# Kernel tuning notes

Measured on AMD Instinct MI355X. Metric: run time of the kernel, lower is better.

The kernel has to match this reference:

```python
import jax, jax.numpy as jnp
import numpy as np

USER_NUM = 100000
ITEM_NUM = 50000
N = USER_NUM + ITEM_NUM
D = 64
NNZ = 2400000
B = 4096
NLEVEL = 3
LEAF = 32
HID = 256
NCLS = 2
NLAYERS = 2
EPS = 0.1
TAU = 0.2


def _l2norm(x, axis=-1):
    return x / jnp.clip(jnp.linalg.norm(x, axis=axis, keepdims=True), 1e-12)


def setup_inputs():
    key = jax.random.key(0)
    ks = jax.random.split(key, 32)
    def w(k, shape):
        fan = shape[-2] if len(shape) >= 2 else shape[-1]
        return jax.random.normal(k, shape, jnp.float32) / np.sqrt(fan)
    z = lambda *s: jnp.zeros(s, jnp.float32)
    return {
        "ego_emb": w(ks[0], (N, D)),
        "gc_w": w(ks[1], (NLAYERS, D, D)), "gc_b": z(NLAYERS, D),
        "bi_w": w(ks[2], (NLAYERS, D, D)), "bi_b": z(NLAYERS, D),
        "uh_w": w(ks[3], (NLEVEL, D, D)), "uh_b": z(NLEVEL, D),
        "ih_w": w(ks[4], (NLEVEL, D, D)), "ih_b": z(NLEVEL, D),
        "ud_w1": w(ks[5], (NLEVEL, D, HID)), "ud_b1": z(NLEVEL, HID),
        "ud_w2": w(ks[6], (NLEVEL, HID, LEAF)), "ud_b2": z(NLEVEL, LEAF),
        "id_w1": w(ks[7], (NLEVEL, D, HID)), "id_b1": z(NLEVEL, HID),
        "id_w2": w(ks[8], (NLEVEL, HID, LEAF)), "id_b2": z(NLEVEL, LEAF),
        "q_w": w(ks[9], (LEAF, LEAF)), "q_b": z(LEAF),
        "k_w": w(ks[10], (LEAF, LEAF)), "k_b": z(LEAF),
        "v_w": w(ks[11], (LEAF, LEAF)), "v_b": z(LEAF),
        "dg_w1": w(ks[12], (NLEVEL * LEAF, D)), "dg_b1": z(D),
        "dg_w2": w(ks[13], (D, D)), "dg_b2": z(D),
        "pr_w": w(ks[14], (D, NCLS)), "pr_b": z(NCLS),
        "adj_vals": jax.random.uniform(ks[15], (NNZ,), jnp.float32) / 16.0,
        "hier_skills": jax.random.uniform(ks[16], (B, NLEVEL * LEAF), jnp.float32),
        "user_id": jax.random.randint(ks[17], (B,), 0, USER_NUM),
        "item_id": jax.random.randint(ks[18], (B,), 0, ITEM_NUM),
        "adj_rows": jax.random.randint(ks[19], (NNZ,), 0, N),
        "adj_cols": jax.random.randint(ks[20], (NNZ,), 0, N),
    }


def _sam(x, q_w, q_b, k_w, k_b, v_w, v_b):
    # x: [B, S, d], single-head self-attention (n_heads=1)
    d = x.shape[-1]
    q = x @ q_w + q_b
    k = x @ k_w + k_b
    v = x @ v_w + v_b
    scores = jnp.einsum('bsd,btd->bst', q, k) / jnp.sqrt(jnp.float32(d))
    attn = jax.nn.softmax(scores, axis=-1)  # softmax over key axis t
    return jnp.einsum('bst,btd->bsd', attn, v)


def _cl_loss(v1, v2):
    n1 = _l2norm(v1)
    n2 = _l2norm(v2)
    pos = jnp.exp(jnp.sum(n1 * n2, -1) / TAU)
    ttl = jnp.sum(jnp.exp(n1 @ n2.T / TAU), axis=1)
    return jnp.mean(-jnp.log(pos / ttl))


def _cl_module(recs, key):
    # recs: [L, B, LEAF]
    noise = jax.random.uniform(key, recs.shape, recs.dtype)
    recs_new = recs + jnp.sign(recs) * _l2norm(noise) * EPS
    return jnp.mean(jax.vmap(_cl_loss)(recs, recs_new))


def reference(ego_emb, gc_w, gc_b, bi_w, bi_b, uh_w, uh_b, ih_w, ih_b,
              ud_w1, ud_b1, ud_w2, ud_b2, id_w1, id_b1, id_w2, id_b2,
              q_w, q_b, k_w, k_b, v_w, v_b, dg_w1, dg_b1, dg_w2, dg_b2,
              pr_w, pr_b, adj_vals, hier_skills, user_id, item_id,
              adj_rows, adj_cols):
    # ---- NGCF propagation: sparse adj matmul + bi-interaction ----
    E = ego_emb
    E_sum = ego_emb
    for l in range(NLAYERS):
        side = jax.ops.segment_sum(adj_vals[:, None] * E[adj_cols], adj_rows,
                                   num_segments=N)  # spmm(adj_norm, E)
        sum_e = jax.nn.leaky_relu(side @ gc_w[l] + gc_b[l])
        bi_e = jax.nn.leaky_relu((E * side) @ bi_w[l] + bi_b[l])
        E = _l2norm(sum_e + bi_e)  # dropout -> identity (eval)
        E_sum = E_sum + E
    ue = E_sum[:USER_NUM][user_id]   # [B, D]
    ie = E_sum[USER_NUM:][item_id]   # [B, D]
    # ---- hierarchy projections + disentangled encoders (stacked over levels) ----
    u_reps = jnp.tanh(jnp.einsum('bd,lde->lbe', ue, uh_w) + uh_b[:, None, :])
    i_reps = jnp.tanh(jnp.einsum('bd,lde->lbe', ie, ih_w) + ih_b[:, None, :])
    u_recs = jnp.einsum('lbh,lhk->lbk',
                        jnp.tanh(jnp.einsum('lbd,ldh->lbh', u_reps, ud_w1) + ud_b1[:, None, :]),
                        ud_w2) + ud_b2[:, None, :]  # [L, B, LEAF]
    i_recs = jnp.einsum('lbh,lhk->lbk',
                        jnp.tanh(jnp.einsum('lbd,ldh->lbh', i_reps, id_w1) + id_b1[:, None, :]),
                        id_w2) + id_b2[:, None, :]
    # ---- self-attention across levels ----
    u_att = _sam(u_recs.transpose(1, 0, 2), q_w, q_b, k_w, k_b, v_w, v_b)  # [B, L, LEAF]
    i_att = _sam(i_recs.transpose(1, 0, 2), q_w, q_b, k_w, k_b, v_w, v_b)
    # ---- contrastive losses (detached in original via torch.Tensor(...)) ----
    kc = jax.random.split(jax.random.key(42), 2)
    cl = _cl_module(u_att.transpose(1, 0, 2), kc[0]) + _cl_module(i_att.transpose(1, 0, 2), kc[1])
    cl = jax.lax.stop_gradient(cl)
    # ---- diagnosis head ----
    skills = hier_skills.reshape(B, NLEVEL, LEAF)
    diag = ((jax.nn.sigmoid(u_att) - jax.nn.sigmoid(i_att)) * skills).reshape(B, NLEVEL * LEAF)
    h = jnp.tanh(diag @ dg_w1 + dg_b1) @ dg_w2 + dg_b2  # dropout -> identity (eval)
    out = jax.nn.softmax(h @ pr_w + pr_b, axis=-1)
    return (out, cl)
```

## Files before the change

kernel.cpp:

```cpp
#include <hip/hip_runtime.h>
#include <stdint.h>
#include <math.h>

#define USER_N 100000
#define NODE_N 150000
#define DD 64
#define NNZE 2400000
#define BB 4096
#define NLV 3
#define LF 32
#define HALF_SZ 196608u
#define NTILE 586
#define NSUB 8
#define SCAP 1024
#define EPB 4096

typedef __attribute__((ext_vector_type(8))) short bf16x8;
typedef __attribute__((ext_vector_type(4))) float f32x4;
typedef __attribute__((ext_vector_type(2))) float f32x2;

#define XCC_ID_IMM 63508

__host__ __device__ inline void tf_block(uint32_t k0, uint32_t k1, uint32_t& x0, uint32_t& x1) {
  uint32_t ks[3] = {k0, k1, k0 ^ k1 ^ 0x1BD11BDAu};
  x0 += ks[0]; x1 += ks[1];
  const int R0[4] = {13, 15, 26, 6};
  const int R1[4] = {17, 29, 16, 24};
#pragma unroll
  for (int i = 0; i < 5; ++i) {
    const int* R = (i & 1) ? R1 : R0;
#pragma unroll
    for (int j = 0; j < 4; ++j) {
      x0 += x1;
      x1 = (x1 << R[j]) | (x1 >> (32 - R[j]));
      x1 ^= x0;
    }
    x0 += ks[(i + 1) % 3];
    x1 += ks[(i + 2) % 3] + (uint32_t)(i + 1);
  }
}

__device__ inline float tf_uniform(uint32_t ka, uint32_t kb, uint32_t m) {
  uint32_t x0, x1;
  bool first = m < HALF_SZ;
  if (first) { x0 = m; x1 = m + HALF_SZ; } else { x0 = m - HALF_SZ; x1 = m; }
  tf_block(ka, kb, x0, x1);
  uint32_t bits = first ? x0 : x1;
  return __uint_as_float((bits >> 9) | 0x3f800000u) - 1.0f;
}

__device__ inline unsigned short f2bf(float x) {
  uint32_t b = __float_as_uint(x);
  return (unsigned short)((b + 0x7FFFu + ((b >> 16) & 1u)) >> 16);
}

__device__ inline unsigned char f2fp8(float x) {
  return (unsigned char)(__builtin_amdgcn_cvt_pk_fp8_f32(x, x, 0, false) & 0xFF);
}

__device__ inline void fp8_fma(float4& acc, uint2 rec, uint32_t wrd) {
  float vv = __uint_as_float(rec.y);
  f32x2 lo = __builtin_amdgcn_cvt_pk_f32_fp8((int)wrd, false);
  f32x2 hi = __builtin_amdgcn_cvt_pk_f32_fp8((int)wrd, true);
  acc.x = fmaf(vv, lo.x, acc.x);
  acc.y = fmaf(vv, lo.y, acc.y);
  acc.z = fmaf(vv, hi.x, acc.z);
  acc.w = fmaf(vv, hi.y, acc.w);
}

__global__ __launch_bounds__(256) void k_init(const float* __restrict__ ego,
                                              uint32_t* __restrict__ E8) {
  int i = blockIdx.x * 256 + threadIdx.x;
  float4 v = ((const float4*)ego)[i];
  int w01 = __builtin_amdgcn_cvt_pk_fp8_f32(v.x, v.y, 0, false);
  int w = __builtin_amdgcn_cvt_pk_fp8_f32(v.z, v.w, w01, true);
  E8[i] = (uint32_t)w;
}

__global__ __launch_bounds__(256) void k_wprep(
    const float* __restrict__ uh_w, const float* __restrict__ ud_w1,
    const float* __restrict__ ud_w2, const float* __restrict__ ih_w,
    const float* __restrict__ id_w1, const float* __restrict__ id_w2,
    unsigned short* __restrict__ s1t, unsigned short* __restrict__ s2t,
    unsigned short* __restrict__ s3t) {
  int i = blockIdx.x * 256 + threadIdx.x;
  if (i < 24576) {
    int sl = i >> 12, r = i & 4095, e = r >> 6, d = r & 63;
    const float* src = (sl >= 3 ? ih_w : uh_w);
    int l = sl % 3;
    s1t[i] = f2bf(src[l * 4096 + d * 64 + e]);
  } else if (i < 24576 + 98304) {
    int j = i - 24576;
    int sl = j >> 14, r = j & 16383, e = r >> 6, d = r & 63;
    const float* src = (sl >= 3 ? id_w1 : ud_w1);
    int l = sl % 3;
    s2t[j] = f2bf(src[l * 16384 + d * 256 + e]);
  } else if (i < 172032) {
    int j = i - 24576 - 98304;
    int sl = j >> 13, r = j & 8191, e = r >> 8, d = r & 255;
    const float* src = (sl >= 3 ? id_w2 : ud_w2);
    int l = sl % 3;
    s3t[j] = f2bf(src[l * 8192 + d * 32 + e]);
  }
}

__global__ __launch_bounds__(256) void k_scatter_t(const int* __restrict__ rows,
                                                   const int* __restrict__ cols,
                                                   const float* __restrict__ vals,
                                                   int* __restrict__ cursor,
                                                   uint2* __restrict__ sedge_r) {
  __shared__ int cnt[NTILE];
  __shared__ int curs[NTILE];
  int t = threadIdx.x;
  for (int i = t; i < NTILE; i += 256) cnt[i] = 0;
  __syncthreads();
  int r[16];
  int ebase = blockIdx.x * EPB;
#pragma unroll
  for (int j = 0; j < 16; ++j) {
    int e = ebase + j * 256 + t;
    r[j] = (e < NNZE) ? rows[e] : -1;
    if (r[j] >= 0) atomicAdd(&cnt[r[j] >> 8], 1);
  }
  __syncthreads();
  unsigned myx = __builtin_amdgcn_s_getreg(XCC_ID_IMM) & (NSUB - 1);
  for (int i = t; i < NTILE; i += 256) {
    int c = cnt[i];
    curs[i] = c ? atomicAdd(&cursor[(i * NSUB + (int)myx) * 16], c) : 0;
  }
  __syncthreads();
#pragma unroll
  for (int j = 0; j < 16; ++j) {
    if (r[j] < 0) continue;
    int e = ebase + j * 256 + t;
    int tile = r[j] >> 8;
    uint2 rec = make_uint2((uint32_t)cols[e] | ((uint32_t)(r[j] & 255) << 18),
                           __float_as_uint(vals[e]));
    int p = atomicAdd(&curs[tile], 1);
    if (p < SCAP) {
      sedge_r[(size_t)(tile * NSUB + (int)myx) * SCAP + p] = rec;
    } else {
#pragma unroll 1
      for (int att = 1; att < NSUB; ++att) {
        int seg = tile * NSUB + (int)((myx + att) & (NSUB - 1));
        int p2 = atomicAdd(&cursor[seg * 16], 1);
        if (p2 < SCAP) { sedge_r[(size_t)seg * SCAP + p2] = rec; break; }
      }
    }
  }
}

__global__ __launch_bounds__(1024) void k_scan586(const int* __restrict__ cursor,
                                                  int* __restrict__ out_base,
                                                  int* __restrict__ row_start) {
  __shared__ int buf[1024];
  int t = threadIdx.x;
  int tot = 0;
  if (t < NTILE) {
#pragma unroll
    for (int x = 0; x < NSUB; ++x) {
      int c = cursor[(t * NSUB + x) * 16];
      tot += (c < SCAP) ? c : SCAP;
    }
  }
  buf[t] = tot;
  __syncthreads();
  for (int off = 1; off < 1024; off <<= 1) {
    int add = (t >= off) ? buf[t - off] : 0;
    __syncthreads();
    buf[t] += add;
    __syncthreads();
  }
  if (t < NTILE) out_base[t] = buf[t] - tot;
  if (t == 0) row_start[NODE_N] = NNZE;
}

__global__ __launch_bounds__(256) void k_sort_t(const uint2* __restrict__ sedge_r,
                                                const int* __restrict__ cursor,
                                                const int* __restrict__ out_base,
                                                uint2* __restrict__ sedge,
                                                int* __restrict__ row_start) {
  __shared__ int hist[256], buf[256], curs[256];
  int t = threadIdx.x;
  int tile = blockIdx.x;
  int obase = out_base[tile];
  hist[t] = 0;
  __syncthreads();
#pragma unroll 1
  for (int x = 0; x < NSUB; ++x) {
    int seg = tile * NSUB + x;
    int cnt = cursor[seg * 16];
    if (cnt > SCAP) cnt = SCAP;
    const uint2* sp = sedge_r + (size_t)seg * SCAP;
    for (int i = t; i < cnt; i += 256)
      atomicAdd(&hist[sp[i].x >> 18], 1);
  }
  __syncthreads();
  int v = hist[t];
  buf[t] = v;
  __syncthreads();
  for (int off = 1; off < 256; off <<= 1) {
    int add = (t >= off) ? buf[t - off] : 0;
    __syncthreads();
    buf[t] += add;
    __syncthreads();
  }
  int excl = buf[t] - v;
  curs[t] = excl;
  int row = tile * 256 + t;
  if (row < NODE_N) row_start[row] = obase + excl;
  __syncthreads();
#pragma unroll 1
  for (int x = 0; x < NSUB; ++x) {
    int seg = tile * NSUB + x;
    int cnt = cursor[seg * 16];
    if (cnt > SCAP) cnt = SCAP;
    const uint2* sp = sedge_r + (size_t)seg * SCAP;
    for (int i = t; i < cnt; i += 256) {
      uint2 rec = sp[i];
      int rl = rec.x >> 18;
      int p = atomicAdd(&curs[rl], 1);
      sedge[obase + p] = make_uint2(rec.x & 0x3FFFFu, rec.y);
    }
  }
}

__global__ __launch_bounds__(256) void k_spmm(const uint32_t* __restrict__ E8,
                                              const uint2* __restrict__ sedge,
                                              const int* __restrict__ row_start,
                                              unsigned short* __restrict__ side16,
                                              unsigned short* __restrict__ p16) {
  int r = blockIdx.x * 4 + (threadIdx.x >> 6);
  int lane = threadIdx.x & 63;
  int g = lane >> 4;
  int q = lane & 15;
  int rs = row_start[r], re = row_start[r + 1];
  float4 acc = make_float4(0.f, 0.f, 0.f, 0.f);
  int e = rs;
  for (; e + 16 <= re; e += 16) {
    uint2 e0 = sedge[e + g];
    uint2 e1 = sedge[e + 4 + g];
    uint2 e2 = sedge[e + 8 + g];
    uint2 e3 = sedge[e + 12 + g];
    uint32_t a0 = E8[(size_t)e0.x * 16 + q];
    uint32_t a1 = E8[(size_t)e1.x * 16 + q];
    uint32_t a2 = E8[(size_t)e2.x * 16 + q];
    uint32_t a3 = E8[(size_t)e3.x * 16 + q];
    fp8_fma(acc, e0, a0);
    fp8_fma(acc, e1, a1);
    fp8_fma(acc, e2, a2);
    fp8_fma(acc, e3, a3);
  }
  for (; e + 8 <= re; e += 8) {
    uint2 e0 = sedge[e + g];
    uint2 e1 = sedge[e + 4 + g];
    uint32_t a0 = E8[(size_t)e0.x * 16 + q];
    uint32_t a1 = E8[(size_t)e1.x * 16 + q];
    fp8_fma(acc, e0, a0);
    fp8_fma(acc, e1, a1);
  }
  for (; e + 4 <= re; e += 4) {
    uint2 e0 = sedge[e + g];
    uint32_t a0 = E8[(size_t)e0.x * 16 + q];
    fp8_fma(acc, e0, a0);
  }
  for (; e < re; ++e) {
    if (g == (e & 3)) {
      uint2 e0 = sedge[e];
      uint32_t a0 = E8[(size_t)e0.x * 16 + q];
      fp8_fma(acc, e0, a0);
    }
  }
#pragma unroll
  for (int off = 16; off <= 32; off <<= 1) {
    acc.x += __shfl_xor(acc.x, off, 64);
    acc.y += __shfl_xor(acc.y, off, 64);
    acc.z += __shfl_xor(acc.z, off, 64);
    acc.w += __shfl_xor(acc.w, off, 64);
  }
  if (g == 0) {
    uint32_t ew = E8[(size_t)r * 16 + q];
    f32x2 elo = __builtin_amdgcn_cvt_pk_f32_fp8((int)ew, false);
    f32x2 ehi = __builtin_amdgcn_cvt_pk_f32_fp8((int)ew, true);
    ushort4 s16, pp;
    s16.x = f2bf(acc.x); s16.y = f2bf(acc.y); s16.z = f2bf(acc.z); s16.w = f2bf(acc.w);
    pp.x = f2bf(acc.x * elo.x); pp.y = f2bf(acc.y * elo.y);
    pp.z = f2bf(acc.z * ehi.x); pp.w = f2bf(acc.w * ehi.y);
    *(ushort4*)&side16[(size_t)r * DD + q * 4] = s16;
    *(ushort4*)&p16[(size_t)r * DD + q * 4] = pp;
  }
}

__global__ __launch_bounds__(256) void k_transform(const float* __restrict__ gw,
                                                   const float* __restrict__ gb,
                                                   const float* __restrict__ bw,
                                                   const float* __restrict__ bb,
                                                   const unsigned short* __restrict__ side16,
                                                   const unsigned short* __restrict__ p16,
                                                   float* __restrict__ Eout,
                                                   unsigned char* __restrict__ E8b) {
  int t = threadIdx.x;
  int wv = t >> 6, lane = t & 63;
  int n = lane & 15, quad = lane >> 4;
  bf16x8 wg[4][2], wb[4][2];
  float gbl[4], bbl[4];
#pragma unroll
  for (int c = 0; c < 4; ++c) {
    gbl[c] = gb[c * 16 + n];
    bbl[c] = bb[c * 16 + n];
#pragma unroll
    for (int h = 0; h < 2; ++h) {
#pragma unroll
      for (int j = 0; j < 8; ++j) {
        int k = h * 32 + quad * 8 + j;
        wg[c][h][j] = (short)f2bf(gw[k * 64 + c * 16 + n]);
        wb[c][h][j] = (short)f2bf(bw[k * 64 + c * 16 + n]);
      }
    }
  }
  const f32x4 z = {0.f, 0.f, 0.f, 0.f};
  for (int tile = blockIdx.x * 4 + wv; tile < NODE_N / 16; tile += gridDim.x * 4) {
    int i0 = tile * 16;
    bf16x8 as0 = *(const bf16x8*)&side16[(size_t)(i0 + n) * DD + quad * 8];
    bf16x8 as1 = *(const bf16x8*)&side16[(size_t)(i0 + n) * DD + 32 + quad * 8];
    bf16x8 ap0 = *(const bf16x8*)&p16[(size_t)(i0 + n) * DD + quad * 8];
    bf16x8 ap1 = *(const bf16x8*)&p16[(size_t)(i0 + n) * DD + 32 + quad * 8];
    float v[4][4];
    float sq0 = 0.f, sq1 = 0.f, sq2 = 0.f, sq3 = 0.f;
#pragma unroll
    for (int c = 0; c < 4; ++c) {
      f32x4 ag = __builtin_amdgcn_mfma_f32_16x16x32_bf16(as0, wg[c][0], z, 0, 0, 0);
      ag = __builtin_amdgcn_mfma_f32_16x16x32_bf16(as1, wg[c][1], ag, 0, 0, 0);
      f32x4 ab = __builtin_amdgcn_mfma_f32_16x16x32_bf16(ap0, wb[c][0], z, 0, 0, 0);
      ab = __builtin_amdgcn_mfma_f32_16x16x32_bf16(ap1, wb[c][1], ab, 0, 0, 0);
#pragma unroll
      for (int r = 0; r < 4; ++r) {
        float a1 = ag[r] + gbl[c];
        a1 = (a1 > 0.f) ? a1 : 0.01f * a1;
        float a2 = ab[r] + bbl[c];
        a2 = (a2 > 0.f) ? a2 : 0.01f * a2;
        float vv = a1 + a2;
        v[c][r] = vv;
        if (r == 0) sq0 += vv * vv;
        else if (r == 1) sq1 += vv * vv;
        else if (r == 2) sq2 += vv * vv;
        else sq3 += vv * vv;
      }
    }
#pragma unroll
    for (int off = 1; off < 16; off <<= 1) {
      sq0 += __shfl_xor(sq0, off, 64);
      sq1 += __shfl_xor(sq1, off, 64);
      sq2 += __shfl_xor(sq2, off, 64);
      sq3 += __shfl_xor(sq3, off, 64);
    }
    float inv0 = 1.f / fmaxf(sqrtf(sq0), 1e-12f);
    float inv1 = 1.f / fmaxf(sqrtf(sq1), 1e-12f);
    float inv2 = 1.f / fmaxf(sqrtf(sq2), 1e-12f);
    float inv3 = 1.f / fmaxf(sqrtf(sq3), 1e-12f);
#pragma unroll
    for (int c = 0; c < 4; ++c) {
      float vn0 = v[c][0] * inv0;
      float vn1 = v[c][1] * inv1;
      float vn2 = v[c][2] * inv2;
      float vn3 = v[c][3] * inv3;
      size_t o0 = (size_t)(i0 + quad * 4 + 0) * DD + c * 16 + n;
      size_t o1 = o0 + DD, o2 = o1 + DD, o3 = o2 + DD;
      Eout[o0] = vn0; Eout[o1] = vn1; Eout[o2] = vn2; Eout[o3] = vn3;
      E8b[o0] = f2fp8(vn0); E8b[o1] = f2fp8(vn1);
      E8b[o2] = f2fp8(vn2); E8b[o3] = f2fp8(vn3);
    }
  }
}

__global__ __launch_bounds__(128) void k_gather(const float* __restrict__ ego,
                                                const float* __restrict__ E1,
                                                const float* __restrict__ E2,
                                                const int* __restrict__ uid,
                                                const int* __restrict__ iid,
                                                unsigned short* __restrict__ ue16,
                                                unsigned short* __restrict__ ie16) {
  int b = blockIdx.x, t = threadIdx.x;
  if (t < 64) {
    size_t o = (size_t)uid[b] * 64 + t;
    ue16[(size_t)b * 64 + t] = f2bf(ego[o] + E1[o] + E2[o]);
  } else {
    int d = t - 64;
    size_t o = (size_t)(USER_N + iid[b]) * 64 + d;
    ie16[(size_t)b * 64 + d] = f2bf(ego[o] + E1[o] + E2[o]);
  }
}

__global__ __launch_bounds__(256) void k_encoder5(
    const unsigned short* __restrict__ ue16, const unsigned short* __restrict__ ie16,
    const unsigned short* __restrict__ s1t, const unsigned short* __restrict__ s2t,
    const unsigned short* __restrict__ s3t,
    const float* __restrict__ uh_b, const float* __restrict__ ud_b1,
    const float* __restrict__ ud_b2, const float* __restrict__ ih_b,
    const float* __restrict__ id_b1, const float* __restrict__ id_b2,
    float* __restrict__ recs_u, float* __restrict__ recs_i) {
  __shared__ unsigned short R1[32][64];
  __shared__ unsigned short T[32][256];
  int t = threadIdx.x;
  int w = t >> 6, lane = t & 63;
  int n = lane & 15, quad = lane >> 4;
  int trow = w & 1;
  int cg = w >> 1;
  int r0 = blockIdx.x * 32;
  int l = blockIdx.y, side = blockIdx.z;
  int sl = side * 3 + l;
  const unsigned short* x16 = side ? ie16 : ue16;
  const float* hb = side ? ih_b : uh_b;
  const float* bb1 = side ? id_b1 : ud_b1;
  const float* bb2 = side ? id_b2 : ud_b2;
  float* recs = side ? recs_i : recs_u;
  const f32x4 z = {0.f, 0.f, 0.f, 0.f};

  {
    const unsigned short* xr = &x16[(size_t)(r0 + trow * 16 + n) * 64];
    bf16x8 a0 = *(const bf16x8*)&xr[quad * 8];
    bf16x8 a1 = *(const bf16x8*)&xr[32 + quad * 8];
    const unsigned short* Wt = s1t + (size_t)sl * 4096;
#pragma unroll
    for (int cc = 0; cc < 2; ++cc) {
      int cb = cg * 2 + cc;
      bf16x8 wb0 = *(const bf16x8*)&Wt[(size_t)(cb * 16 + n) * 64 + quad * 8];
      bf16x8 wb1 = *(const bf16x8*)&Wt[(size_t)(cb * 16 + n) * 64 + 32 + quad * 8];
      f32x4 acc = __builtin_amdgcn_mfma_f32_16x16x32_bf16(a0, wb0, z, 0, 0, 0);
      acc = __builtin_amdgcn_mfma_f32_16x16x32_bf16(a1, wb1, acc, 0, 0, 0);
      float bias = hb[l * 64 + cb * 16 + n];
#pragma unroll
      for (int r = 0; r < 4; ++r)
        R1[trow * 16 + quad * 4 + r][cb * 16 + n] = f2bf(tanhf(acc[r] + bias));
    }
  }
  __syncthreads();

  {
    bf16x8 a0 = *(const bf16x8*)&R1[trow * 16 + n][quad * 8];
    bf16x8 a1 = *(const bf16x8*)&R1[trow * 16 + n][32 + quad * 8];
    const unsigned short* Wt = s2t + (size_t)sl * 16384;
#pragma unroll
    for (int cc = 0; cc < 8; ++cc) {
      int cb = cg * 8 + cc;
      bf16x8 wb0 = *(const bf16x8*)&Wt[(size_t)(cb * 16 + n) * 64 + quad * 8];
      bf16x8 wb1 = *(const bf16x8*)&Wt[(size_t)(cb * 16 + n) * 64 + 32 + quad * 8];
      f32x4 acc = __builtin_amdgcn_mfma_f32_16x16x32_bf16(a0, wb0, z, 0, 0, 0);
      acc = __builtin_amdgcn_mfma_f32_16x16x32_bf16(a1, wb1, acc, 0, 0, 0);
      float bias = bb1[l * 256 + cb * 16 + n];
#pragma unroll
      for (int r = 0; r < 4; ++r)
        T[trow * 16 + quad * 4 + r][cb * 16 + n] = f2bf(tanhf(acc[r] + bias));
    }
  }
  __syncthreads();

  {
    const unsigned short* Wt = s3t + (size_t)sl * 8192;
    f32x4 acc = z;
#pragma unroll
    for (int h = 0; h < 8; ++h) {
      bf16x8 a = *(const bf16x8*)&T[trow * 16 + n][h * 32 + quad * 8];
      bf16x8 b = *(const bf16x8*)&Wt[(size_t)(cg * 16 + n) * 256 + h * 32 + quad * 8];
      acc = __builtin_amdgcn_mfma_f32_16x16x32_bf16(a, b, acc, 0, 0, 0);
    }
    float bias = bb2[l * 32 + cg * 16 + n];
#pragma unroll
    for (int r = 0; r < 4; ++r)
      recs[((size_t)l * BB + (r0 + trow * 16 + quad * 4 + r)) * 32 + cg * 16 + n] =
          acc[r] + bias;
  }
}

__global__ __launch_bounds__(256) void k_attn(const float* __restrict__ recs,
                                              const float* __restrict__ qw, const float* __restrict__ qb,
                                              const float* __restrict__ kw, const float* __restrict__ kb,
                                              const float* __restrict__ vw, const float* __restrict__ vb,
                                              float* __restrict__ att) {
  int t = threadIdx.x;
  int b = blockIdx.x * 8 + (t >> 5);
  int d = t & 31;
  float x0 = recs[((size_t)0 * BB + b) * 32 + d];
  float x1 = recs[((size_t)1 * BB + b) * 32 + d];
  float x2 = recs[((size_t)2 * BB + b) * 32 + d];
  float q0 = qb[d], q1 = q0, q2 = q0;
  float c0 = kb[d], c1 = c0, c2 = c0;
  float v0 = vb[d], v1 = v0, v2 = v0;
#pragma unroll 4
  for (int kk = 0; kk < 32; ++kk) {
    float xa = __shfl(x0, kk, 32);
    float xb = __shfl(x1, kk, 32);
    float xc = __shfl(x2, kk, 32);
    float wq = qw[kk * 32 + d], wk = kw[kk * 32 + d], wv = vw[kk * 32 + d];
    q0 += xa * wq; q1 += xb * wq; q2 += xc * wq;
    c0 += xa * wk; c1 += xb * wk; c2 += xc * wk;
    v0 += xa * wv; v1 += xb * wv; v2 += xc * wv;
  }
  float qs[3] = {q0, q1, q2}, ks[3] = {c0, c1, c2}, vs[3] = {v0, v1, v2};
  float sc[3][3];
#pragma unroll
  for (int s = 0; s < 3; ++s)
#pragma unroll
    for (int u = 0; u < 3; ++u) {
      float p = qs[s] * ks[u];
#pragma unroll
      for (int off = 16; off; off >>= 1) p += __shfl_xor(p, off, 32);
      sc[s][u] = p * 0.17677669529663687f;
    }
#pragma unroll
  for (int s = 0; s < 3; ++s) {
    float m = fmaxf(sc[s][0], fmaxf(sc[s][1], sc[s][2]));
    float e0 = __expf(sc[s][0] - m), e1 = __expf(sc[s][1] - m), e2 = __expf(sc[s][2] - m);
    float inv = 1.f / (e0 + e1 + e2);
    att[(size_t)b * 96 + s * 32 + d] = (e0 * vs[0] + e1 * vs[1] + e2 * vs[2]) * inv;
  }
}

__global__ __launch_bounds__(256) void k_noise(const float* __restrict__ att_u,
                                               const float* __restrict__ att_i,
                                               uint32_t ku0, uint32_t ku1, uint32_t ki0, uint32_t ki1,
                                               unsigned short* __restrict__ n1b,
                                               unsigned short* __restrict__ n2b,
                                               float* __restrict__ posdot) {
  int t = threadIdx.x;
  int g = blockIdx.x * 8 + (t >> 5);
  int k = t & 31;
  int side = g / (NLV * BB);
  int rem = g - side * (NLV * BB);
  int l = rem >> 12;
  int b = rem & 4095;
  const float* att = side ? att_i : att_u;
  uint32_t ka = side ? ki0 : ku0;
  uint32_t kb = side ? ki1 : ku1;
  float r = att[(size_t)b * 96 + l * 32 + k];
  float ss = r * r;
#pragma unroll
  for (int off = 16; off; off >>= 1) ss += __shfl_xor(ss, off, 32);
  float v1 = r / fmaxf(sqrtf(ss), 1e-12f);
  uint32_t m = ((uint32_t)(l * BB + b)) * 32u + (uint32_t)k;
  float u = tf_uniform(ka, kb, m);
  float us = u * u;
#pragma unroll
  for (int off = 16; off; off >>= 1) us += __shfl_xor(us, off, 32);
  float un = u / fmaxf(sqrtf(us), 1e-12f);
  float sgn = (r > 0.f) ? 1.f : ((r < 0.f) ? -1.f : 0.f);
  float rn = r + sgn * un * 0.1f;
  float s2 = rn * rn;
#pragma unroll
  for (int off = 16; off; off >>= 1) s2 += __shfl_xor(s2, off, 32);
  float v2 = rn / fmaxf(sqrtf(s2), 1e-12f);
  float pd = v1 * v2;
#pragma unroll
  for (int off = 16; off; off >>= 1) pd += __shfl_xor(pd, off, 32);
  size_t o = (size_t)g * 32 + k;
  n1b[o] = f2bf(v1);
  n2b[o] = f2bf(v2);
  if (k == 0) posdot[g] = pd;
}

__global__ __launch_bounds__(256) void k_ttl(const unsigned short* __restrict__ n1b,
                                             const unsigned short* __restrict__ n2b,
                                             float* __restrict__ ttl) {
  int t = threadIdx.x;
  int wv = t >> 6, lane = t & 63;
  int sl = blockIdx.x >> 6;
  int istripe = blockIdx.x & 63;
  int i0 = istripe * 64 + wv * 16;
  const unsigned short* ab = n1b + (size_t)sl * BB * 32;
  const unsigned short* bb = n2b + (size_t)sl * BB * 32;
  int m = lane & 15, quad = lane >> 4;
  bf16x8 afrag = *(const bf16x8*)&ab[(size_t)(i0 + m) * 32 + quad * 8];
  float r0a = 0.f, r1a = 0.f, r2a = 0.f, r3a = 0.f;
  f32x4 z = {0.f, 0.f, 0.f, 0.f};
  for (int jt = 0; jt < 256; jt += 4) {
    bf16x8 b0 = *(const bf16x8*)&bb[((size_t)((jt + 0) * 16 + m)) * 32 + quad * 8];
    bf16x8 b1 = *(const bf16x8*)&bb[((size_t)((jt + 1) * 16 + m)) * 32 + quad * 8];
    bf16x8 b2 = *(const bf16x8*)&bb[((size_t)((jt + 2) * 16 + m)) * 32 + quad * 8];
    bf16x8 b3 = *(const bf16x8*)&bb[((size_t)((jt + 3) * 16 + m)) * 32 + quad * 8];
    f32x4 s0 = __builtin_amdgcn_mfma_f32_16x16x32_bf16(afrag, b0, z, 0, 0, 0);
    f32x4 s1 = __builtin_amdgcn_mfma_f32_16x16x32_bf16(afrag, b1, z, 0, 0, 0);
    f32x4 s2 = __builtin_amdgcn_mfma_f32_16x16x32_bf16(afrag, b2, z, 0, 0, 0);
    f32x4 s3 = __builtin_amdgcn_mfma_f32_16x16x32_bf16(afrag, b3, z, 0, 0, 0);
    r0a += __expf(s0.x * 5.f) + __expf(s1.x * 5.f) + __expf(s2.x * 5.f) + __expf(s3.x * 5.f);
    r1a += __expf(s0.y * 5.f) + __expf(s1.y * 5.f) + __expf(s2.y * 5.f) + __expf(s3.y * 5.f);
    r2a += __expf(s0.z * 5.f) + __expf(s1.z * 5.f) + __expf(s2.z * 5.f) + __expf(s3.z * 5.f);
    r3a += __expf(s0.w * 5.f) + __expf(s1.w * 5.f) + __expf(s2.w * 5.f) + __expf(s3.w * 5.f);
  }
#pragma unroll
  for (int off = 1; off < 16; off <<= 1) {
    r0a += __shfl_xor(r0a, off, 64);
    r1a += __shfl_xor(r1a, off, 64);
    r2a += __shfl_xor(r2a, off, 64);
    r3a += __shfl_xor(r3a, off, 64);
  }
  if (m == 0) {
    int rbase = sl * BB + i0 + quad * 4;
    ttl[rbase + 0] = r0a;
    ttl[rbase + 1] = r1a;
    ttl[rbase + 2] = r2a;
    ttl[rbase + 3] = r3a;
  }
}

__global__ __launch_bounds__(1024) void k_clred(const float* __restrict__ ttl,
                                                const float* __restrict__ posdot,
                                                float* __restrict__ outp) {
  __shared__ float red[1024];
  int t = threadIdx.x;
  float a = 0.f;
  for (int idx = t; idx < 6 * BB; idx += 1024)
    a += logf(ttl[idx]) - posdot[idx] * 5.0f;
  red[t] = a;
  __syncthreads();
  for (int off = 512; off; off >>= 1) {
    if (t < off) red[t] += red[t + off];
    __syncthreads();
  }
  if (t == 0) outp[2 * BB] = red[0] * (1.f / 12288.f);
}

__global__ __launch_bounds__(256) void k_head(const float* __restrict__ att_u,
                                              const float* __restrict__ att_i,
                                              const float* __restrict__ skills,
                                              const float* __restrict__ w1, const float* __restrict__ b1,
                                              const float* __restrict__ w2, const float* __restrict__ b2,
                                              const float* __restrict__ pw, const float* __restrict__ pb,
                                              float* __restrict__ outp) {
  __shared__ float diag[4][96], t1[4][64];
  int t = threadIdx.x;
  int w = t >> 6, lane = t & 63;
  int b = blockIdx.x * 4 + w;
  for (int j = lane; j < 96; j += 64) {
    float su = 1.f / (1.f + __expf(-att_u[(size_t)b * 96 + j]));
    float si = 1.f / (1.f + __expf(-att_i[(size_t)b * 96 + j]));
    diag[w][j] = (su - si) * skills[(size_t)b * 96 + j];
  }
  __syncthreads();
  float a = b1[lane];
#pragma unroll 8
  for (int j = 0; j < 96; ++j) a += diag[w][j] * w1[j * 64 + lane];
  t1[w][lane] = tanhf(a);
  __syncthreads();
  float h = b2[lane];
#pragma unroll 8
  for (int kk = 0; kk < 64; ++kk) h += t1[w][kk] * w2[kk * 64 + lane];
  float p0 = h * pw[lane * 2 + 0];
  float p1 = h * pw[lane * 2 + 1];
#pragma unroll
  for (int off = 32; off; off >>= 1) {
    p0 += __shfl_xor(p0, off, 64);
    p1 += __shfl_xor(p1, off, 64);
  }
  if (lane == 0) {
    float l0 = p0 + pb[0], l1 = p1 + pb[1];
    float m = fmaxf(l0, l1);
    float e0 = __expf(l0 - m), e1 = __expf(l1 - m);
    float inv = 1.f / (e0 + e1);
    outp[(size_t)b * 2 + 0] = e0 * inv;
    outp[(size_t)b * 2 + 1] = e1 * inv;
  }
}

extern "C" void kernel_launch(void* const* d_in, const int* in_sizes, int n_in,
                              void* d_out, int out_size, void* d_ws, size_t ws_size,
                              hipStream_t stream) {
  const float* ego    = (const float*)d_in[0];
  const float* gc_w   = (const float*)d_in[1];
  const float* gc_b   = (const float*)d_in[2];
  const float* bi_w   = (const float*)d_in[3];
  const float* bi_b   = (const float*)d_in[4];
  const float* uh_w   = (const float*)d_in[5];
  const float* uh_b   = (const float*)d_in[6];
  const float* ih_w   = (const float*)d_in[7];
  const float* ih_b   = (const float*)d_in[8];
  const float* ud_w1  = (const float*)d_in[9];
  const float* ud_b1  = (const float*)d_in[10];
  const float* ud_w2  = (const float*)d_in[11];
  const float* ud_b2  = (const float*)d_in[12];
  const float* id_w1  = (const float*)d_in[13];
  const float* id_b1  = (const float*)d_in[14];
  const float* id_w2  = (const float*)d_in[15];
  const float* id_b2  = (const float*)d_in[16];
  const float* q_w    = (const float*)d_in[17];
  const float* q_b    = (const float*)d_in[18];
  const float* k_w    = (const float*)d_in[19];
  const float* k_b    = (const float*)d_in[20];
  const float* v_w    = (const float*)d_in[21];
  const float* v_b    = (const float*)d_in[22];
  const float* dg_w1  = (const float*)d_in[23];
  const float* dg_b1  = (const float*)d_in[24];
  const float* dg_w2  = (const float*)d_in[25];
  const float* dg_b2  = (const float*)d_in[26];
  const float* pr_w   = (const float*)d_in[27];
  const float* pr_b   = (const float*)d_in[28];
  const float* adj_vals = (const float*)d_in[29];
  const float* skills = (const float*)d_in[30];
  const int* user_id  = (const int*)d_in[31];
  const int* item_id  = (const int*)d_in[32];
  const int* adj_rows = (const int*)d_in[33];
  const int* adj_cols = (const int*)d_in[34];
  float* outp = (float*)d_out;

  char* w = (char*)d_ws;
  auto alloc = [&](size_t bytes) -> char* {
    char* p = w;
    w += (bytes + 255) & ~(size_t)255;
    return p;
  };
  float* E1     = (float*)alloc((size_t)NODE_N * DD * 4);
  float* E2     = (float*)alloc((size_t)NODE_N * DD * 4);
  uint32_t* E8  = (uint32_t*)alloc((size_t)NODE_N * DD);
  unsigned short* side16 = (unsigned short*)alloc((size_t)NODE_N * DD * 2);
  unsigned short* p16    = (unsigned short*)alloc((size_t)NODE_N * DD * 2);
  uint2* sedge_r= (uint2*)alloc((size_t)NTILE * NSUB * SCAP * 8);
  uint2* sedge  = (uint2*)alloc((size_t)NNZE * 8);
  int*   cursor = (int*)  alloc((size_t)NTILE * NSUB * 16 * 4);
  int*   out_base = (int*)alloc((size_t)(NTILE + 1) * 4);
  int*   row_start = (int*)alloc((size_t)(NODE_N + 1) * 4);
  float* posdot = (float*)alloc((size_t)6 * BB * 4);
  float* ttl    = (float*)alloc((size_t)6 * BB * 4);
  unsigned short* s1t = (unsigned short*)alloc((size_t)24576 * 2);
  unsigned short* s2t = (unsigned short*)alloc((size_t)98304 * 2);
  unsigned short* s3t = (unsigned short*)alloc((size_t)49152 * 2);

  char* ap = (char*)sedge_r;
  auto alias = [&](size_t bytes) -> char* {
    char* p = ap;
    ap += (bytes + 255) & ~(size_t)255;
    return p;
  };
  unsigned short* ue16 = (unsigned short*)alias((size_t)BB * 64 * 2);
  unsigned short* ie16 = (unsigned short*)alias((size_t)BB * 64 * 2);
  float* recs_u = (float*)alias((size_t)NLV * BB * 32 * 4);
  float* recs_i = (float*)alias((size_t)NLV * BB * 32 * 4);
  float* att_u  = (float*)alias((size_t)BB * 96 * 4);
  float* att_i  = (float*)alias((size_t)BB * 96 * 4);
  unsigned short* n1b = (unsigned short*)alias((size_t)6 * BB * 32 * 2);
  unsigned short* n2b = (unsigned short*)alias((size_t)6 * BB * 32 * 2);

  uint32_t a0 = 0, a1 = 2, b0 = 1, b1 = 3;
  tf_block(0u, 42u, a0, a1);
  tf_block(0u, 42u, b0, b1);
  uint32_t ku0 = a0, ku1 = b0;
  uint32_t ki0 = a1, ki1 = b1;

  (void)hipMemsetAsync(cursor, 0, (size_t)NTILE * NSUB * 16 * 4, stream);

  k_init<<<9375, 256, 0, stream>>>(ego, E8);
  k_wprep<<<672, 256, 0, stream>>>(uh_w, ud_w1, ud_w2, ih_w, id_w1, id_w2,
                                   s1t, s2t, s3t);
  k_scatter_t<<<(NNZE + EPB - 1) / EPB, 256, 0, stream>>>(adj_rows, adj_cols, adj_vals,
                                                          cursor, sedge_r);
  k_scan586<<<1, 1024, 0, stream>>>(cursor, out_base, row_start);
  k_sort_t<<<NTILE, 256, 0, stream>>>(sedge_r, cursor, out_base, sedge, row_start);

  float* Ebufs[2] = {E1, E2};
  for (int l = 0; l < 2; ++l) {
    k_spmm<<<37500, 256, 0, stream>>>(E8, sedge, row_start, side16, p16);
    k_transform<<<1172, 256, 0, stream>>>(gc_w + l * 4096, gc_b + l * 64,
                                          bi_w + l * 4096, bi_b + l * 64,
                                          side16, p16, Ebufs[l], (unsigned char*)E8);
  }

  k_gather<<<4096, 128, 0, stream>>>(ego, E1, E2, user_id, item_id, ue16, ie16);

  dim3 ge(128, 3, 2);
  k_encoder5<<<ge, 256, 0, stream>>>(ue16, ie16, s1t, s2t, s3t,
                                     uh_b, ud_b1, ud_b2, ih_b, id_b1, id_b2,
                                     recs_u, recs_i);

  k_attn<<<512, 256, 0, stream>>>(recs_u, q_w, q_b, k_w, k_b, v_w, v_b, att_u);
  k_attn<<<512, 256, 0, stream>>>(recs_i, q_w, q_b, k_w, k_b, v_w, v_b, att_i);

  k_noise<<<3072, 256, 0, stream>>>(att_u, att_i, ku0, ku1, ki0, ki1, n1b, n2b, posdot);

  k_ttl<<<384, 256, 0, stream>>>(n1b, n2b, ttl);
  k_clred<<<1, 1024, 0, stream>>>(ttl, posdot, outp);

  k_head<<<1024, 256, 0, stream>>>(att_u, att_i, skills, dg_w1, dg_b1, dg_w2, dg_b2,
                                   pr_w, pr_b, outp);
}
```

Measured before the change: 559.8 us.

## Merge init/wprep and attn launches, fold tile scan into sort, stage sorted edges in LDS

Merges k_init and k_wprep into one launch and batches the two k_attn launches into a single 2D grid, cutting launch count. The single-block prefix scan kernel is removed: each sort tile now computes its own output base by summing all earlier segment counts and combining them with a shared atomic. Sorted edges are staged in a 40KB LDS buffer and written out contiguously, with direct writes as a fallback when a tile overflows. This trades redundant cursor reads (later tiles read up to ~4.7K counts) and higher LDS use for fewer launches and coalesced stores.

```diff
diff --git a/kernel.cpp b/kernel.cpp
--- a/kernel.cpp
+++ b/kernel.cpp
@@ -14,6 +14,7 @@
 #define NSUB 8
 #define SCAP 1024
 #define EPB 4096
+#define LCAP 5120
 
 typedef __attribute__((ext_vector_type(8))) short bf16x8;
 typedef __attribute__((ext_vector_type(4))) float f32x4;
@@ -68,22 +69,22 @@
   acc.w = fmaf(vv, hi.y, acc.w);
 }
 
-__global__ __launch_bounds__(256) void k_init(const float* __restrict__ ego,
-                                              uint32_t* __restrict__ E8) {
-  int i = blockIdx.x * 256 + threadIdx.x;
-  float4 v = ((const float4*)ego)[i];
-  int w01 = __builtin_amdgcn_cvt_pk_fp8_f32(v.x, v.y, 0, false);
-  int w = __builtin_amdgcn_cvt_pk_fp8_f32(v.z, v.w, w01, true);
-  E8[i] = (uint32_t)w;
-}
-
-__global__ __launch_bounds__(256) void k_wprep(
+__global__ __launch_bounds__(256) void k_init(
+    const float* __restrict__ ego, uint32_t* __restrict__ E8,
     const float* __restrict__ uh_w, const float* __restrict__ ud_w1,
     const float* __restrict__ ud_w2, const float* __restrict__ ih_w,
     const float* __restrict__ id_w1, const float* __restrict__ id_w2,
     unsigned short* __restrict__ s1t, unsigned short* __restrict__ s2t,
     unsigned short* __restrict__ s3t) {
-  int i = blockIdx.x * 256 + threadIdx.x;
+  if (blockIdx.x < 9375) {
+    int i = blockIdx.x * 256 + threadIdx.x;
+    float4 v = ((const float4*)ego)[i];
+    int w01 = __builtin_amdgcn_cvt_pk_fp8_f32(v.x, v.y, 0, false);
+    int w = __builtin_amdgcn_cvt_pk_fp8_f32(v.z, v.w, w01, true);
+    E8[i] = (uint32_t)w;
+    return;
+  }
+  int i = (blockIdx.x - 9375) * 256 + threadIdx.x;
   if (i < 24576) {
     int sl = i >> 12, r = i & 4095, e = r >> 6, d = r & 63;
     const float* src = (sl >= 3 ? ih_w : uh_w);
@@ -150,52 +151,38 @@
   }
 }
 
-__global__ __launch_bounds__(1024) void k_scan586(const int* __restrict__ cursor,
-                                                  int* __restrict__ out_base,
-                                                  int* __restrict__ row_start) {
-  __shared__ int buf[1024];
-  int t = threadIdx.x;
-  int tot = 0;
-  if (t < NTILE) {
-#pragma unroll
-    for (int x = 0; x < NSUB; ++x) {
-      int c = cursor[(t * NSUB + x) * 16];
-      tot += (c < SCAP) ? c : SCAP;
-    }
-  }
-  buf[t] = tot;
-  __syncthreads();
-  for (int off = 1; off < 1024; off <<= 1) {
-    int add = (t >= off) ? buf[t - off] : 0;
-    __syncthreads();
-    buf[t] += add;
-    __syncthreads();
-  }
-  if (t < NTILE) out_base[t] = buf[t] - tot;
-  if (t == 0) row_start[NODE_N] = NNZE;
-}
-
 __global__ __launch_bounds__(256) void k_sort_t(const uint2* __restrict__ sedge_r,
                                                 const int* __restrict__ cursor,
-                                                const int* __restrict__ out_base,
                                                 uint2* __restrict__ sedge,
                                                 int* __restrict__ row_start) {
   __shared__ int hist[256], buf[256], curs[256];
+  __shared__ int obase_s;
+  __shared__ uint2 staged[LCAP];
   int t = threadIdx.x;
   int tile = blockIdx.x;
-  int obase = out_base[tile];
+  if (t == 0) obase_s = 0;
   hist[t] = 0;
   __syncthreads();
+  int ob = 0;
+  for (int i = t; i < tile * NSUB; i += 256) {
+    int c = cursor[i * 16];
+    ob += (c < SCAP) ? c : SCAP;
+  }
+  if (ob) atomicAdd(&obase_s, ob);
+  int segcnt[NSUB];
+#pragma unroll
+  for (int x = 0; x < NSUB; ++x) {
+    int c = cursor[(tile * NSUB + x) * 16];
+    segcnt[x] = (c < SCAP) ? c : SCAP;
+  }
 #pragma unroll 1
   for (int x = 0; x < NSUB; ++x) {
-    int seg = tile * NSUB + x;
-    int cnt = cursor[seg * 16];
-    if (cnt > SCAP) cnt = SCAP;
-    const uint2* sp = sedge_r + (size_t)seg * SCAP;
-    for (int i = t; i < cnt; i += 256)
+    const uint2* sp = sedge_r + (size_t)(tile * NSUB + x) * SCAP;
+    for (int i = t; i < segcnt[x]; i += 256)
       atomicAdd(&hist[sp[i].x >> 18], 1);
   }
   __syncthreads();
+  int obase = obase_s;
   int v = hist[t];
   buf[t] = v;
   __syncthreads();
@@ -205,24 +192,29 @@
     buf[t] += add;
     __syncthreads();
   }
+  int total = buf[255];
   int excl = buf[t] - v;
   curs[t] = excl;
   int row = tile * 256 + t;
   if (row < NODE_N) row_start[row] = obase + excl;
+  if (tile == NTILE - 1 && t == 0) row_start[NODE_N] = NNZE;
   __syncthreads();
 #pragma unroll 1
   for (int x = 0; x < NSUB; ++x) {
-    int seg = tile * NSUB + x;
-    int cnt = cursor[seg * 16];
-    if (cnt > SCAP) cnt = SCAP;
-    const uint2* sp = sedge_r + (size_t)seg * SCAP;
-    for (int i = t; i < cnt; i += 256) {
+    const uint2* sp = sedge_r + (size_t)(tile * NSUB + x) * SCAP;
+    for (int i = t; i < segcnt[x]; i += 256) {
       uint2 rec = sp[i];
       int rl = rec.x >> 18;
       int p = atomicAdd(&curs[rl], 1);
-      sedge[obase + p] = make_uint2(rec.x & 0x3FFFFu, rec.y);
-    }
-  }
+      uint2 outrec = make_uint2(rec.x & 0x3FFFFu, rec.y);
+      if (p < LCAP) staged[p] = outrec;
+      else sedge[obase + p] = outrec;
+    }
+  }
+  __syncthreads();
+  int n = (total < LCAP) ? total : LCAP;
+  for (int i = t; i < n; i += 256)
+    sedge[obase + i] = staged[i];
 }
 
 __global__ __launch_bounds__(256) void k_spmm(const uint32_t* __restrict__ E8,
@@ -472,11 +464,15 @@
   }
 }
 
-__global__ __launch_bounds__(256) void k_attn(const float* __restrict__ recs,
+__global__ __launch_bounds__(256) void k_attn(const float* __restrict__ recs_u,
+                                              const float* __restrict__ recs_i,
                                               const float* __restrict__ qw, const float* __restrict__ qb,
                                               const float* __restrict__ kw, const float* __restrict__ kb,
                                               const float* __restrict__ vw, const float* __restrict__ vb,
-                                              float* __restrict__ att) {
+                                              float* __restrict__ att_u,
+                                              float* __restrict__ att_i) {
+  const float* recs = blockIdx.y ? recs_i : recs_u;
+  float* att = blockIdx.y ? att_i : att_u;
   int t = threadIdx.x;
   int b = blockIdx.x * 8 + (t >> 5);
   int d = t & 31;
@@ -715,7 +711,6 @@
   uint2* sedge_r= (uint2*)alloc((size_t)NTILE * NSUB * SCAP * 8);
   uint2* sedge  = (uint2*)alloc((size_t)NNZE * 8);
   int*   cursor = (int*)  alloc((size_t)NTILE * NSUB * 16 * 4);
-  int*   out_base = (int*)alloc((size_t)(NTILE + 1) * 4);
   int*   row_start = (int*)alloc((size_t)(NODE_N + 1) * 4);
   float* posdot = (float*)alloc((size_t)6 * BB * 4);
   float* ttl    = (float*)alloc((size_t)6 * BB * 4);
@@ -746,13 +741,11 @@
 
   (void)hipMemsetAsync(cursor, 0, (size_t)NTILE * NSUB * 16 * 4, stream);
 
-  k_init<<<9375, 256, 0, stream>>>(ego, E8);
-  k_wprep<<<672, 256, 0, stream>>>(uh_w, ud_w1, ud_w2, ih_w, id_w1, id_w2,
-                                   s1t, s2t, s3t);
+  k_init<<<9375 + 672, 256, 0, stream>>>(ego, E8, uh_w, ud_w1, ud_w2,
+                                         ih_w, id_w1, id_w2, s1t, s2t, s3t);
   k_scatter_t<<<(NNZE + EPB - 1) / EPB, 256, 0, stream>>>(adj_rows, adj_cols, adj_vals,
                                                           cursor, sedge_r);
-  k_scan586<<<1, 1024, 0, stream>>>(cursor, out_base, row_start);
-  k_sort_t<<<NTILE, 256, 0, stream>>>(sedge_r, cursor, out_base, sedge, row_start);
+  k_sort_t<<<NTILE, 256, 0, stream>>>(sedge_r, cursor, sedge, row_start);
 
   float* Ebufs[2] = {E1, E2};
   for (int l = 0; l < 2; ++l) {
@@ -769,8 +762,9 @@
                                      uh_b, ud_b1, ud_b2, ih_b, id_b1, id_b2,
                                      recs_u, recs_i);
 
-  k_attn<<<512, 256, 0, stream>>>(recs_u, q_w, q_b, k_w, k_b, v_w, v_b, att_u);
-  k_attn<<<512, 256, 0, stream>>>(recs_i, q_w, q_b, k_w, k_b, v_w, v_b, att_i);
+  dim3 ga(512, 2);
+  k_attn<<<ga, 256, 0, stream>>>(recs_u, recs_i, q_w, q_b, k_w, k_b, v_w, v_b,
+                                 att_u, att_i);
 
   k_noise<<<3072, 256, 0, stream>>>(att_u, att_i, ku0, ku1, ki0, ki1, n1b, n2b, posdot);
 
```

Result: faster. 540.6 us (-3.4%).
